# Performance work log

Measured on AMD Instinct MI355X. Metric: run time of the kernel, lower is better.

The kernel has to match this reference:

```python
import jax, jax.numpy as jnp
import numpy as np

B, S, H, A = 16, 2048, 512, 256


def setup_inputs() -> dict:
    key = jax.random.key(0)
    k1, k2, k3 = jax.random.split(key, 3)
    x = jax.random.normal(k1, (B, S, H), dtype=jnp.float32)
    W_a = jax.random.normal(k2, (A, H), dtype=jnp.float32) * (1.0 / np.sqrt(H))
    q = jax.random.normal(k3, (1, A), dtype=jnp.float32) * (1.0 / np.sqrt(A))
    return {"x": x, "W_a": W_a, "q": q}


def reference(x, W_a, q):
    # x: [B,S,H], W_a: [A,H], q: [1,A]
    Bm, Sm, Hm = x.shape
    # Per-key score e[b,t] = q . tanh(W_a @ x[b,t]).
    # In the original, keys for t > s are zeroed BEFORE the bias-free linear;
    # tanh(0)=0 and the -inf softmax mask removes those entries, so the score
    # is independent of the query position s -> no O(S^2*H*A) recompute needed.
    e = jnp.einsum('oa,bta->bt', q, jnp.tanh(jnp.einsum('bth,ah->bta', x, W_a)))  # [B,S]
    causal = jnp.where(jnp.tril(jnp.ones((Sm, Sm), dtype=bool)), 0.0, -jnp.inf)  # [S_query, S_key]
    logits = e[:, None, :] + causal[None, :, :]            # [B,S,S]
    d = jax.nn.softmax(logits, axis=-1)                    # attention over keys t<=s
    # masked values v_masked[b,s,t,:] = [t<=s]*x[b,t,:]; d is already 0 for t>s
    a = jnp.einsum('bst,bth->bsh', d, x)                   # [B,S,H]
    return a[:, :, None, :], d[:, :, None, :]              # [B,S,1,H], [B,S,1,S] as in torch
```

## Files before the change

### kernel.cpp

```cpp
#include <hip/hip_runtime.h>
#include <hip/hip_bf16.h>
#include <math.h>

#define BB 16
#define SS 2048
#define HH 512
#define AA 256
#define NCH 64
#define CT  (SS/NCH)
#define XST 72

typedef short bf16x8 __attribute__((ext_vector_type(8)));
typedef float f32x4  __attribute__((ext_vector_type(4)));

__device__ __forceinline__ short f2bf(float f) {
    union { __hip_bfloat16 h; short s; } u;
    u.h = __float2bfloat16(f);
    return u.s;
}

__device__ __forceinline__ void nt_store4(float4 v, float4* p) {
    f32x4 o = {v.x, v.y, v.z, v.w};
    __builtin_nontemporal_store(o, (f32x4*)p);
}

__global__ __launch_bounds__(256) void convW_kernel(
    const float* __restrict__ W, short* __restrict__ Wb)
{
    int i = blockIdx.x * 256 + threadIdx.x;
    float4 v = ((const float4*)W)[i];
    short4 o = make_short4(f2bf(v.x), f2bf(v.y), f2bf(v.z), f2bf(v.w));
    ((short4*)Wb)[i] = o;
}

__global__ __launch_bounds__(256, 2) void gemm_e_mfma(
    const float* __restrict__ x, const short* __restrict__ Wb,
    const float* __restrict__ q, float* __restrict__ e)
{
    __shared__ short Xl[64 * XST];
    __shared__ short Wl[256 * XST];
    __shared__ float epart[2][64];

    const int tid  = threadIdx.x;
    const int lane = tid & 63;
    const int wv   = tid >> 6;
    const int wm   = wv & 1;
    const int wn   = wv >> 1;
    const int quad = lane >> 4;
    const int col  = lane & 15;
    const long tok0 = (long)blockIdx.x * 64;

    f32x4 acc[2][8];
    #pragma unroll
    for (int mt = 0; mt < 2; mt++)
        #pragma unroll
        for (int nt = 0; nt < 8; nt++) acc[mt][nt] = (f32x4){0.f, 0.f, 0.f, 0.f};

    for (int kc = 0; kc < HH; kc += 64) {
        __syncthreads();
        #pragma unroll
        for (int i = 0; i < 2; i++) {
            int task = i * 256 + tid;
            int row = task >> 3, seg = task & 7;
            const float* src = &x[(tok0 + row) * HH + kc + seg * 8];
            float4 v0 = *(const float4*)src;
            float4 v1 = *(const float4*)(src + 4);
            bf16x8 o;
            o[0] = f2bf(v0.x); o[1] = f2bf(v0.y); o[2] = f2bf(v0.z); o[3] = f2bf(v0.w);
            o[4] = f2bf(v1.x); o[5] = f2bf(v1.y); o[6] = f2bf(v1.z); o[7] = f2bf(v1.w);
            *(bf16x8*)&Xl[row * XST + seg * 8] = o;
        }
        #pragma unroll
        for (int i = 0; i < 8; i++) {
            int task = i * 256 + tid;
            int row = task >> 3, seg = task & 7;
            bf16x8 v = *(const bf16x8*)&Wb[row * HH + kc + seg * 8];
            *(bf16x8*)&Wl[row * XST + seg * 8] = v;
        }
        __syncthreads();
        #pragma unroll
        for (int kk = 0; kk < 64; kk += 32) {
            bf16x8 af[2], bfr[8];
            #pragma unroll
            for (int mt = 0; mt < 2; mt++)
                af[mt] = *(bf16x8*)&Xl[(wm * 32 + mt * 16 + col) * XST + kk + quad * 8];
            #pragma unroll
            for (int nt = 0; nt < 8; nt++)
                bfr[nt] = *(bf16x8*)&Wl[(wn * 128 + nt * 16 + col) * XST + kk + quad * 8];
            #pragma unroll
            for (int mt = 0; mt < 2; mt++)
                #pragma unroll
                for (int nt = 0; nt < 8; nt++)
                    acc[mt][nt] = __builtin_amdgcn_mfma_f32_16x16x32_bf16(
                        af[mt], bfr[nt], acc[mt][nt], 0, 0, 0);
        }
    }

    float qv[8];
    #pragma unroll
    for (int nt = 0; nt < 8; nt++) qv[nt] = q[wn * 128 + nt * 16 + col];
    #pragma unroll
    for (int mt = 0; mt < 2; mt++) {
        #pragma unroll
        for (int reg = 0; reg < 4; reg++) {
            float sv = 0.f;
            #pragma unroll
            for (int nt = 0; nt < 8; nt++) sv += qv[nt] * tanhf(acc[mt][nt][reg]);
            #pragma unroll
            for (int off = 1; off < 16; off <<= 1) sv += __shfl_xor(sv, off, 64);
            if (col == 0)
                epart[wn][wm * 32 + mt * 16 + quad * 4 + reg] = sv;
        }
    }
    __syncthreads();
    if (tid < 64) e[tok0 + tid] = epart[0][tid] + epart[1][tid];
}

__global__ __launch_bounds__(256) void softmax_scan_kernel(
    const float* __restrict__ e, float* __restrict__ w, float* __restrict__ zinv)
{
    __shared__ float wmax[4];
    __shared__ float wsum[4];
    const int b = blockIdx.x, tid = threadIdx.x;
    const int lane = tid & 63, wvi = tid >> 6;
    const float* eb = e + b * SS;
    float v[8];
    #pragma unroll
    for (int j = 0; j < 8; j++) v[j] = eb[tid * 8 + j];
    float m = v[0];
    #pragma unroll
    for (int j = 1; j < 8; j++) m = fmaxf(m, v[j]);
    #pragma unroll
    for (int off = 32; off > 0; off >>= 1) m = fmaxf(m, __shfl_xor(m, off, 64));
    if (lane == 0) wmax[wvi] = m;
    __syncthreads();
    const float mb = fmaxf(fmaxf(wmax[0], wmax[1]), fmaxf(wmax[2], wmax[3]));
    float we[8], pf[8], p = 0.f;
    #pragma unroll
    for (int j = 0; j < 8; j++) { we[j] = expf(v[j] - mb); p += we[j]; pf[j] = p; }
    float incl = p;
    #pragma unroll
    for (int off = 1; off < 64; off <<= 1) {
        float t = __shfl_up(incl, off, 64);
        if (lane >= off) incl += t;
    }
    if (lane == 63) wsum[wvi] = incl;
    __syncthreads();
    float base = 0.f;
    for (int ww = 0; ww < wvi; ww++) base += wsum[ww];
    const float excl = base + incl - p;
    #pragma unroll
    for (int j = 0; j < 8; j++) {
        float Z = excl + pf[j];
        w[b * SS + tid * 8 + j]    = we[j];
        zinv[b * SS + tid * 8 + j] = 1.0f / Z;
    }
}

__global__ __launch_bounds__(256) void write_d_kernel(
    const float* __restrict__ w, const float* __restrict__ zinv,
    float* __restrict__ dout)
{
    const int blk = blockIdx.x;
    const int b  = blk >> 7;
    const int sg = blk & 127;
    const int s0 = sg << 4;
    const int tid = threadIdx.x;
    const float4* wb = (const float4*)(w + b * SS);
    const float4 wa = wb[tid];
    const float4 wc = wb[tid + 256];
    const int ta = tid * 4;
    const int tc = (tid + 256) * 4;
    const float* zb = zinv + b * SS + s0;
    float4* rowbase = (float4*)(dout + (size_t)(b * SS + s0) * SS);
    #pragma unroll
    for (int r = 0; r < 16; r++) {
        const int s = s0 + r;
        const float zi = zb[r];
        float4 oa, oc;
        oa.x = (ta + 0 <= s) ? wa.x * zi : 0.f;
        oa.y = (ta + 1 <= s) ? wa.y * zi : 0.f;
        oa.z = (ta + 2 <= s) ? wa.z * zi : 0.f;
        oa.w = (ta + 3 <= s) ? wa.w * zi : 0.f;
        oc.x = (tc + 0 <= s) ? wc.x * zi : 0.f;
        oc.y = (tc + 1 <= s) ? wc.y * zi : 0.f;
        oc.z = (tc + 2 <= s) ? wc.z * zi : 0.f;
        oc.w = (tc + 3 <= s) ? wc.w * zi : 0.f;
        nt_store4(oa, rowbase + (size_t)r * (SS / 4) + tid);
        nt_store4(oc, rowbase + (size_t)r * (SS / 4) + tid + 256);
    }
}

__global__ __launch_bounds__(128) void scan_part_kernel(
    const float* __restrict__ x, const float* __restrict__ w, float* __restrict__ P)
{
    const int blk = blockIdx.x;
    const int b = blk >> 6;
    const int c = blk & (NCH - 1);
    const int tid = threadIdx.x;
    const int t0 = c * CT;
    const float4* xb = (const float4*)(x + ((size_t)b * SS + t0) * HH);
    const float* wb = w + b * SS + t0;
    float4 acc = make_float4(0.f, 0.f, 0.f, 0.f);
    #pragma unroll 4
    for (int t = 0; t < CT; t++) {
        float wt = wb[t];
        float4 xv = xb[(size_t)t * (HH / 4) + tid];
        acc.x = fmaf(wt, xv.x, acc.x);
        acc.y = fmaf(wt, xv.y, acc.y);
        acc.z = fmaf(wt, xv.z, acc.z);
        acc.w = fmaf(wt, xv.w, acc.w);
    }
    ((float4*)P)[(size_t)blk * (HH / 4) + tid] = acc;
}

__global__ __launch_bounds__(128) void scan_emit_kernel(
    const float* __restrict__ x, const float* __restrict__ w,
    const float* __restrict__ zinv, const float* __restrict__ P,
    float* __restrict__ aout)
{
    const int blk = blockIdx.x;
    const int b = blk >> 6;
    const int c = blk & (NCH - 1);
    const int tid = threadIdx.x;
    const float4* Pb = (const float4*)P + (size_t)b * NCH * (HH / 4) + tid;
    float4 base = make_float4(0.f, 0.f, 0.f, 0.f);
    for (int cc = 0; cc < c; cc++) {
        float4 p = Pb[(size_t)cc * (HH / 4)];
        base.x += p.x; base.y += p.y; base.z += p.z; base.w += p.w;
    }
    const int t0 = c * CT;
    const float4* xb = (const float4*)(x + ((size_t)b * SS + t0) * HH);
    const float* wb = w + b * SS + t0;
    const float* zb = zinv + b * SS + t0;
    float4* ab = (float4*)(aout + ((size_t)b * SS + t0) * HH);
    #pragma unroll 4
    for (int t = 0; t < CT; t++) {
        float wt = wb[t];
        float zi = zb[t];
        float4 xv = xb[(size_t)t * (HH / 4) + tid];
        base.x = fmaf(wt, xv.x, base.x);
        base.y = fmaf(wt, xv.y, base.y);
        base.z = fmaf(wt, xv.z, base.z);
        base.w = fmaf(wt, xv.w, base.w);
        float4 o = make_float4(base.x * zi, base.y * zi, base.z * zi, base.w * zi);
        nt_store4(o, &ab[(size_t)t * (HH / 4) + tid]);
    }
}

extern "C" void kernel_launch(void* const* d_in, const int* in_sizes, int n_in,
                              void* d_out, int out_size, void* d_ws, size_t ws_size,
                              hipStream_t stream)
{
    const float* x = (const float*)d_in[0];
    const float* W = (const float*)d_in[1];
    const float* q = (const float*)d_in[2];
    float* out  = (float*)d_out;
    float* aout = out;
    float* dout = out + (size_t)BB * SS * HH;

    float* ws   = (float*)d_ws;
    float* e    = ws;
    float* w    = ws + BB * SS;
    float* zinv = ws + 2 * BB * SS;
    float* P    = ws + 3 * BB * SS;
    short* Wb   = (short*)(ws + 3 * BB * SS + BB * NCH * HH);

    hipLaunchKernelGGL(convW_kernel, dim3(AA * HH / 4 / 256), dim3(256), 0, stream,
                       W, Wb);
    hipLaunchKernelGGL(gemm_e_mfma, dim3(BB * SS / 64), dim3(256), 0, stream,
                       x, Wb, q, e);
    hipLaunchKernelGGL(softmax_scan_kernel, dim3(BB), dim3(256), 0, stream,
                       e, w, zinv);
    hipLaunchKernelGGL(write_d_kernel, dim3(BB * SS / 16), dim3(256), 0, stream,
                       w, zinv, dout);
    hipLaunchKernelGGL(scan_part_kernel, dim3(BB * NCH), dim3(128), 0, stream,
                       x, w, P);
    hipLaunchKernelGGL(scan_emit_kernel, dim3(BB * NCH), dim3(128), 0, stream,
                       x, w, zinv, P, aout);
}
```

Baseline: 436.3 us.

## Fuse d-matrix write with chunk partial sums and precompute chunk prefixes

Merges the d-output writer and the per-chunk partial-sum kernel into one launch: extra blocks compute partial sums of w*x while the other blocks stream out the large d matrix. A new single-pass kernel turns the chunk partial sums into exclusive prefixes, so the emit kernel reads one base vector instead of looping over all earlier chunks. The chunk count doubles, giving more emit blocks with shorter serial scans. In exchange it adds a launch and a small serial prefix kernel with only 16 blocks.

Result: no change. 437.1 us (+0.2%).

```diff
diff --git a/kernel.cpp b/kernel.cpp
--- a/kernel.cpp
+++ b/kernel.cpp
@@ -6,7 +6,7 @@
 #define SS 2048
 #define HH 512
 #define AA 256
-#define NCH 64
+#define NCH 128
 #define CT  (SS/NCH)
 #define XST 72
 
@@ -157,61 +157,83 @@
     }
 }
 
-__global__ __launch_bounds__(256) void write_d_kernel(
+__global__ __launch_bounds__(256) void fused_d_part_kernel(
     const float* __restrict__ w, const float* __restrict__ zinv,
-    float* __restrict__ dout)
+    const float* __restrict__ x, float* __restrict__ dout,
+    float* __restrict__ P)
 {
     const int blk = blockIdx.x;
-    const int b  = blk >> 7;
-    const int sg = blk & 127;
-    const int s0 = sg << 4;
     const int tid = threadIdx.x;
-    const float4* wb = (const float4*)(w + b * SS);
-    const float4 wa = wb[tid];
-    const float4 wc = wb[tid + 256];
-    const int ta = tid * 4;
-    const int tc = (tid + 256) * 4;
-    const float* zb = zinv + b * SS + s0;
-    float4* rowbase = (float4*)(dout + (size_t)(b * SS + s0) * SS);
-    #pragma unroll
-    for (int r = 0; r < 16; r++) {
-        const int s = s0 + r;
-        const float zi = zb[r];
-        float4 oa, oc;
-        oa.x = (ta + 0 <= s) ? wa.x * zi : 0.f;
-        oa.y = (ta + 1 <= s) ? wa.y * zi : 0.f;
-        oa.z = (ta + 2 <= s) ? wa.z * zi : 0.f;
-        oa.w = (ta + 3 <= s) ? wa.w * zi : 0.f;
-        oc.x = (tc + 0 <= s) ? wc.x * zi : 0.f;
-        oc.y = (tc + 1 <= s) ? wc.y * zi : 0.f;
-        oc.z = (tc + 2 <= s) ? wc.z * zi : 0.f;
-        oc.w = (tc + 3 <= s) ? wc.w * zi : 0.f;
-        nt_store4(oa, rowbase + (size_t)r * (SS / 4) + tid);
-        nt_store4(oc, rowbase + (size_t)r * (SS / 4) + tid + 256);
-    }
-}
-
-__global__ __launch_bounds__(128) void scan_part_kernel(
-    const float* __restrict__ x, const float* __restrict__ w, float* __restrict__ P)
-{
-    const int blk = blockIdx.x;
-    const int b = blk >> 6;
-    const int c = blk & (NCH - 1);
-    const int tid = threadIdx.x;
-    const int t0 = c * CT;
-    const float4* xb = (const float4*)(x + ((size_t)b * SS + t0) * HH);
-    const float* wb = w + b * SS + t0;
-    float4 acc = make_float4(0.f, 0.f, 0.f, 0.f);
-    #pragma unroll 4
-    for (int t = 0; t < CT; t++) {
-        float wt = wb[t];
-        float4 xv = xb[(size_t)t * (HH / 4) + tid];
-        acc.x = fmaf(wt, xv.x, acc.x);
-        acc.y = fmaf(wt, xv.y, acc.y);
-        acc.z = fmaf(wt, xv.z, acc.z);
-        acc.w = fmaf(wt, xv.w, acc.w);
-    }
-    ((float4*)P)[(size_t)blk * (HH / 4) + tid] = acc;
+    if (blk < BB * SS / 16) {
+        const int b  = blk >> 7;
+        const int sg = blk & 127;
+        const int s0 = sg << 4;
+        const float4* wb = (const float4*)(w + b * SS);
+        const float4 wa = wb[tid];
+        const float4 wc = wb[tid + 256];
+        const int ta = tid * 4;
+        const int tc = (tid + 256) * 4;
+        const float* zb = zinv + b * SS + s0;
+        float4* rowbase = (float4*)(dout + (size_t)(b * SS + s0) * SS);
+        #pragma unroll
+        for (int r = 0; r < 16; r++) {
+            const int s = s0 + r;
+            const float zi = zb[r];
+            float4 oa, oc;
+            oa.x = (ta + 0 <= s) ? wa.x * zi : 0.f;
+            oa.y = (ta + 1 <= s) ? wa.y * zi : 0.f;
+            oa.z = (ta + 2 <= s) ? wa.z * zi : 0.f;
+            oa.w = (ta + 3 <= s) ? wa.w * zi : 0.f;
+            oc.x = (tc + 0 <= s) ? wc.x * zi : 0.f;
+            oc.y = (tc + 1 <= s) ? wc.y * zi : 0.f;
+            oc.z = (tc + 2 <= s) ? wc.z * zi : 0.f;
+            oc.w = (tc + 3 <= s) ? wc.w * zi : 0.f;
+            nt_store4(oa, rowbase + (size_t)r * (SS / 4) + tid);
+            nt_store4(oc, rowbase + (size_t)r * (SS / 4) + tid + 256);
+        }
+    } else {
+        const int vb = blk - BB * SS / 16;
+        const int b  = vb >> 6;
+        const int cp = vb & 63;
+        const int g   = tid >> 7;
+        const int col = tid & 127;
+        const int c   = cp * 2 + g;
+        const int t0  = c * CT;
+        const float4* xb = (const float4*)(x + ((size_t)b * SS + t0) * HH);
+        const float* wb = w + b * SS + t0;
+        float4 acc = make_float4(0.f, 0.f, 0.f, 0.f);
+        #pragma unroll
+        for (int t = 0; t < CT; t++) {
+            float wt = wb[t];
+            float4 xv = xb[(size_t)t * (HH / 4) + col];
+            acc.x = fmaf(wt, xv.x, acc.x);
+            acc.y = fmaf(wt, xv.y, acc.y);
+            acc.z = fmaf(wt, xv.z, acc.z);
+            acc.w = fmaf(wt, xv.w, acc.w);
+        }
+        ((float4*)P)[((size_t)b * NCH + c) * (HH / 4) + col] = acc;
+    }
+}
+
+__global__ __launch_bounds__(128) void chunk_prefix_kernel(float* __restrict__ P)
+{
+    const int b = blockIdx.x, tid = threadIdx.x;
+    float4* Pb = (float4*)P + (size_t)b * NCH * (HH / 4) + tid;
+    float4 run = make_float4(0.f, 0.f, 0.f, 0.f);
+    for (int c = 0; c < NCH; c += 4) {
+        float4 p0 = Pb[(size_t)(c + 0) * (HH / 4)];
+        float4 p1 = Pb[(size_t)(c + 1) * (HH / 4)];
+        float4 p2 = Pb[(size_t)(c + 2) * (HH / 4)];
+        float4 p3 = Pb[(size_t)(c + 3) * (HH / 4)];
+        Pb[(size_t)(c + 0) * (HH / 4)] = run;
+        run.x += p0.x; run.y += p0.y; run.z += p0.z; run.w += p0.w;
+        Pb[(size_t)(c + 1) * (HH / 4)] = run;
+        run.x += p1.x; run.y += p1.y; run.z += p1.z; run.w += p1.w;
+        Pb[(size_t)(c + 2) * (HH / 4)] = run;
+        run.x += p2.x; run.y += p2.y; run.z += p2.z; run.w += p2.w;
+        Pb[(size_t)(c + 3) * (HH / 4)] = run;
+        run.x += p3.x; run.y += p3.y; run.z += p3.z; run.w += p3.w;
+    }
 }
 
 __global__ __launch_bounds__(128) void scan_emit_kernel(
@@ -220,15 +242,10 @@
     float* __restrict__ aout)
 {
     const int blk = blockIdx.x;
-    const int b = blk >> 6;
+    const int b = blk >> 7;
     const int c = blk & (NCH - 1);
     const int tid = threadIdx.x;
-    const float4* Pb = (const float4*)P + (size_t)b * NCH * (HH / 4) + tid;
-    float4 base = make_float4(0.f, 0.f, 0.f, 0.f);
-    for (int cc = 0; cc < c; cc++) {
-        float4 p = Pb[(size_t)cc * (HH / 4)];
-        base.x += p.x; base.y += p.y; base.z += p.z; base.w += p.w;
-    }
+    float4 base = ((const float4*)P)[(size_t)blk * (HH / 4) + tid];
     const int t0 = c * CT;
     const float4* xb = (const float4*)(x + ((size_t)b * SS + t0) * HH);
     const float* wb = w + b * SS + t0;
@@ -272,10 +289,10 @@
                        x, Wb, q, e);
     hipLaunchKernelGGL(softmax_scan_kernel, dim3(BB), dim3(256), 0, stream,
                        e, w, zinv);
-    hipLaunchKernelGGL(write_d_kernel, dim3(BB * SS / 16), dim3(256), 0, stream,
-                       w, zinv, dout);
-    hipLaunchKernelGGL(scan_part_kernel, dim3(BB * NCH), dim3(128), 0, stream,
-                       x, w, P);
+    hipLaunchKernelGGL(fused_d_part_kernel, dim3(BB * SS / 16 + BB * NCH / 2), dim3(256), 0, stream,
+                       w, zinv, x, dout, P);
+    hipLaunchKernelGGL(chunk_prefix_kernel, dim3(BB), dim3(128), 0, stream,
+                       P);
     hipLaunchKernelGGL(scan_emit_kernel, dim3(BB * NCH), dim3(128), 0, stream,
                        x, w, zinv, P, aout);
 }
```
